# Kernel optimization log

Measured on AMD Instinct MI355X. Metric: run time of the kernel, lower is better.

## Reference

```python
import jax, jax.numpy as jnp
import numpy as np

N_NODE = 50000
N_EDGE = 625000
FDIM = 128
HID = 128
EPS = 1e-5


def setup_inputs() -> dict:
    key = jax.random.key(0)
    ks = jax.random.split(key, 12)
    node_feature = jax.random.normal(ks[0], (N_NODE, FDIM), dtype=jnp.float32)
    edge_matrix = jax.random.randint(ks[1], (2, N_EDGE), 0, N_NODE, dtype=jnp.int32)
    edge_feature = jax.random.normal(ks[2], (N_EDGE, FDIM), dtype=jnp.float32)
    in_dim = FDIM + FDIM  # concat(node, aggregated edge)
    s1 = 1.0 / np.sqrt(in_dim)
    s2 = 1.0 / np.sqrt(HID)
    W1 = jax.random.uniform(ks[3], (in_dim, HID), jnp.float32, -s1, s1)
    b1 = jax.random.uniform(ks[4], (HID,), jnp.float32, -s1, s1)
    W2 = jax.random.uniform(ks[5], (HID, HID), jnp.float32, -s2, s2)
    b2 = jax.random.uniform(ks[6], (HID,), jnp.float32, -s2, s2)
    W3 = jax.random.uniform(ks[7], (HID, FDIM), jnp.float32, -s2, s2)
    b3 = jax.random.uniform(ks[8], (FDIM,), jnp.float32, -s2, s2)
    gamma = jnp.ones((FDIM,), jnp.float32)
    beta = jnp.zeros((FDIM,), jnp.float32)
    return {"node_feature": node_feature, "edge_matrix": edge_matrix,
            "edge_feature": edge_feature, "W1": W1, "b1": b1, "W2": W2,
            "b2": b2, "W3": W3, "b3": b3, "gamma": gamma, "beta": beta}


def reference(node_feature, edge_matrix, edge_feature, W1, b1, W2, b2, W3, b3, gamma, beta):
    # receiver_idx = edge_matrix.T[:, 1] with edge_matrix [2, N_edge] -> row 1
    receiver_idx = edge_matrix[1]
    # scatter_add over receiver: [N_node, fdim]
    agg = jax.ops.segment_sum(edge_feature, receiver_idx, num_segments=node_feature.shape[0])
    x = jnp.concatenate([node_feature, agg], axis=-1)  # [N_node, 2*fdim]
    h = jax.nn.relu(x @ W1 + b1)
    h = jax.nn.relu(h @ W2 + b2)
    h = h @ W3 + b3
    # LayerNorm over last dim (eps = 1e-5, torch default)
    mu = jnp.mean(h, axis=-1, keepdims=True)
    var = jnp.mean((h - mu) ** 2, axis=-1, keepdims=True)
    h = (h - mu) * jax.lax.rsqrt(var + EPS) * gamma + beta
    return h + node_feature
```

## Files before the change

kernel.cpp:

```cpp
#include <hip/hip_runtime.h>
#include <hip/hip_bf16.h>

#define N_NODE 50000
#define N_EDGE 625000
#define FDIM 128
#define CAP 64

typedef __bf16 bf16x8 __attribute__((ext_vector_type(8)));
typedef float floatx4 __attribute__((ext_vector_type(4)));

#define MT 64
#define XS_LD 264
#define H_LD 136

__device__ inline bf16x8 as_bf16x8(uint4 v) {
    union { uint4 u; bf16x8 b; } c; c.u = v; return c.b;
}

__global__ __launch_bounds__(256) void wrepack_kernel(
    const float* __restrict__ W1, const float* __restrict__ W2,
    const float* __restrict__ W3, uint4* __restrict__ wp,
    int* __restrict__ count)
{
    if (blockIdx.x >= 32) {
        int idx = (blockIdx.x - 32) * 256 + threadIdx.x;
        for (int i = idx; i < N_NODE; i += 32 * 256) count[i] = 0;
        return;
    }
    int g = blockIdx.x * 256 + threadIdx.x;
    int lane = g & 63;
    int nt = (g >> 6) & 7;
    int tile = g >> 9;
    const float* W; int k0;
    if (tile < 8)       { W = W1; k0 = tile * 32; }
    else if (tile < 12) { W = W2; k0 = (tile - 8) * 32; }
    else                { W = W3; k0 = (tile - 12) * 32; }
    int n = nt * 16 + (lane & 15);
    int kb = k0 + (lane >> 4) * 8;
    union { __bf16 b[8]; uint4 u; } p;
#pragma unroll
    for (int j = 0; j < 8; ++j) p.b[j] = (__bf16)W[(kb + j) * 128 + n];
    wp[g] = p.u;
}

__global__ __launch_bounds__(256) void scatter_kernel(
    const int4* __restrict__ recv4, int* __restrict__ count, int* __restrict__ eid)
{
    int tid = blockIdx.x * 256 + threadIdx.x;
    if (tid < N_EDGE / 4) {
        int4 r = recv4[tid];
        int e0 = tid * 4;
        int p0 = atomicAdd(&count[r.x], 1);
        int p1 = atomicAdd(&count[r.y], 1);
        int p2 = atomicAdd(&count[r.z], 1);
        int p3 = atomicAdd(&count[r.w], 1);
        if (p0 < CAP) eid[(r.x << 6) + p0] = e0;
        if (p1 < CAP) eid[(r.y << 6) + p1] = e0 + 1;
        if (p2 < CAP) eid[(r.z << 6) + p2] = e0 + 2;
        if (p3 < CAP) eid[(r.w << 6) + p3] = e0 + 3;
    }
}

__global__ __launch_bounds__(256) void gather_kernel(
    const float4* __restrict__ ef4, const int* __restrict__ count,
    const int* __restrict__ eid, uint2* __restrict__ agg)
{
    int wave = threadIdx.x >> 6;
    int lane = threadIdx.x & 63;
    int node = blockIdx.x * 4 + wave;
    int half = lane >> 5;
    int c = lane & 31;
    float4 acc = {0.f, 0.f, 0.f, 0.f};
    int ids = eid[(node << 6) + lane];
    int cnt = count[node]; if (cnt > CAP) cnt = CAP;
    int j = 0;
    for (; j + 8 <= cnt; j += 8) {
        int ea = __shfl(ids, j + half);
        int eb = __shfl(ids, j + 2 + half);
        int ec = __shfl(ids, j + 4 + half);
        int ed = __shfl(ids, j + 6 + half);
        float4 va = ef4[(long)ea * 32 + c];
        float4 vb = ef4[(long)eb * 32 + c];
        float4 vc = ef4[(long)ec * 32 + c];
        float4 vd = ef4[(long)ed * 32 + c];
        acc.x += va.x + vb.x + vc.x + vd.x;
        acc.y += va.y + vb.y + vc.y + vd.y;
        acc.z += va.z + vb.z + vc.z + vd.z;
        acc.w += va.w + vb.w + vc.w + vd.w;
    }
    if (j + 4 <= cnt) {
        int ea = __shfl(ids, j + half);
        int eb = __shfl(ids, j + 2 + half);
        float4 va = ef4[(long)ea * 32 + c];
        float4 vb = ef4[(long)eb * 32 + c];
        acc.x += va.x + vb.x; acc.y += va.y + vb.y;
        acc.z += va.z + vb.z; acc.w += va.w + vb.w;
        j += 4;
    }
    if (j + 2 <= cnt) {
        int e = __shfl(ids, j + half);
        float4 v = ef4[(long)e * 32 + c];
        acc.x += v.x; acc.y += v.y; acc.z += v.z; acc.w += v.w;
        j += 2;
    }
    if (j + half < cnt) {
        int e = __shfl(ids, j + half);
        float4 v = ef4[(long)e * 32 + c];
        acc.x += v.x; acc.y += v.y; acc.z += v.z; acc.w += v.w;
    }
    acc.x += __shfl_xor(acc.x, 32);
    acc.y += __shfl_xor(acc.y, 32);
    acc.z += __shfl_xor(acc.z, 32);
    acc.w += __shfl_xor(acc.w, 32);
    if (half == 0) {
        union { __bf16 b[4]; uint2 u; } p;
        p.b[0] = (__bf16)acc.x; p.b[1] = (__bf16)acc.y;
        p.b[2] = (__bf16)acc.z; p.b[3] = (__bf16)acc.w;
        agg[(long)node * 32 + c] = p.u;
    }
}

__global__ __launch_bounds__(256, 4) void mlp_kernel(
    const float* __restrict__ nodef, const int* __restrict__ agg32,
    const uint4* __restrict__ wp,
    const float* __restrict__ b1, const float* __restrict__ b2,
    const float* __restrict__ b3,
    const float* __restrict__ gamma, const float* __restrict__ beta,
    float* __restrict__ out)
{
    __shared__ __bf16 smem[17472];
    __bf16* xs = smem;
    __bf16* h1 = smem;
    __bf16* h2 = smem + 8704;

    const int t = threadIdx.x;
    const int wave = t >> 6;
    const int lane = t & 63;
    const int quad = lane >> 4;
    const int l16 = lane & 15;
    const int w16 = wave << 4;
    const int q8 = quad << 3;
    const int node0 = blockIdx.x * MT;

    const float4* nf4 = (const float4*)nodef;
#pragma unroll
    for (int i = 0; i < 8; ++i) {
        int it = i * 256 + t;
        int row = it >> 5;
        int c4 = it & 31;
        int node = node0 + row;
        if (node >= N_NODE) node = N_NODE - 1;
        float4 v = nf4[(long)node * 32 + c4];
        union { __bf16 b[4]; short4 s; } u;
        u.b[0] = (__bf16)v.x; u.b[1] = (__bf16)v.y;
        u.b[2] = (__bf16)v.z; u.b[3] = (__bf16)v.w;
        *(short4*)&xs[row * XS_LD + c4 * 4] = u.s;
    }
    const int4* ag4 = (const int4*)agg32;
#pragma unroll
    for (int i = 0; i < 4; ++i) {
        int it = i * 256 + t;
        int row = it >> 4;
        int c8 = it & 15;
        int node = node0 + row;
        if (node >= N_NODE) node = N_NODE - 1;
        int4 v = ag4[(long)node * 16 + c8];
        *(int4*)&xs[row * XS_LD + 128 + c8 * 8] = v;
    }

    floatx4 acc[8];
    const floatx4 zero = {0.f, 0.f, 0.f, 0.f};

    auto run_gemm = [&](const __bf16* A, int ldA, const uint4* __restrict__ wpt, int nk) {
#pragma unroll
        for (int nt = 0; nt < 8; ++nt) acc[nt] = zero;
        const __bf16* arow = A + (w16 + l16) * ldA + q8;
        bf16x8 a = *(const bf16x8*)arow;
        bf16x8 bA[4], bB[4];
#pragma unroll
        for (int i = 0; i < 4; ++i) bA[i] = as_bf16x8(wpt[i * 64 + lane]);
        for (int kc = 0; kc < nk; ++kc) {
            const uint4* wk = wpt + kc * 512;
#pragma unroll
            for (int i = 0; i < 4; ++i) bB[i] = as_bf16x8(wk[(4 + i) * 64 + lane]);
            bf16x8 a2 = a;
            if (kc + 1 < nk) a2 = *(const bf16x8*)(arow + (kc + 1) * 32);
#pragma unroll
            for (int nt = 0; nt < 4; ++nt)
                acc[nt] = __builtin_amdgcn_mfma_f32_16x16x32_bf16(a, bA[nt], acc[nt], 0, 0, 0);
            if (kc + 1 < nk) {
#pragma unroll
                for (int i = 0; i < 4; ++i) bA[i] = as_bf16x8(wk[512 + i * 64 + lane]);
            }
#pragma unroll
            for (int nt = 0; nt < 4; ++nt)
                acc[4 + nt] = __builtin_amdgcn_mfma_f32_16x16x32_bf16(a, bB[nt], acc[4 + nt], 0, 0, 0);
            a = a2;
        }
    };

    auto epilogue_relu = [&](const float* __restrict__ bias, __bf16* H) {
#pragma unroll
        for (int nt = 0; nt < 8; ++nt) {
            int col = nt * 16 + l16;
            float bv = bias[col];
#pragma unroll
            for (int r = 0; r < 4; ++r) {
                float v = acc[nt][r] + bv;
                v = v > 0.f ? v : 0.f;
                H[(w16 + quad * 4 + r) * H_LD + col] = (__bf16)v;
            }
        }
    };

    __syncthreads();
    run_gemm(xs, XS_LD, wp, 8);
    __syncthreads();
    epilogue_relu(b1, h1);
    __syncthreads();
    run_gemm(h1, H_LD, wp + 4096, 4);
    epilogue_relu(b2, h2);
    __syncthreads();
    run_gemm(h2, H_LD, wp + 6144, 4);

    float vout[8][4];
    float sum[4] = {0.f, 0.f, 0.f, 0.f};
    float sq[4]  = {0.f, 0.f, 0.f, 0.f};
#pragma unroll
    for (int nt = 0; nt < 8; ++nt) {
        int col = nt * 16 + l16;
        float bv = b3[col];
#pragma unroll
        for (int r = 0; r < 4; ++r) {
            float v = acc[nt][r] + bv;
            vout[nt][r] = v;
            sum[r] += v;
            sq[r] += v * v;
        }
    }
#pragma unroll
    for (int r = 0; r < 4; ++r) {
#pragma unroll
        for (int offs = 1; offs < 16; offs <<= 1) {
            sum[r] += __shfl_xor(sum[r], offs);
            sq[r]  += __shfl_xor(sq[r], offs);
        }
    }
    float mu[4], rs[4];
#pragma unroll
    for (int r = 0; r < 4; ++r) {
        mu[r] = sum[r] * (1.f / 128.f);
        float var = sq[r] * (1.f / 128.f) - mu[r] * mu[r];
        rs[r] = rsqrtf(var + 1e-5f);
    }
#pragma unroll
    for (int nt = 0; nt < 8; ++nt) {
        int col = nt * 16 + l16;
        float g = gamma[col], be = beta[col];
#pragma unroll
        for (int r = 0; r < 4; ++r) {
            int row = w16 + quad * 4 + r;
            int node = node0 + row;
            if (node < N_NODE) {
                long o = (long)node * 128 + col;
                out[o] = (vout[nt][r] - mu[r]) * rs[r] * g + be + nodef[o];
            }
        }
    }
}

extern "C" void kernel_launch(void* const* d_in, const int* in_sizes, int n_in,
                              void* d_out, int out_size, void* d_ws, size_t ws_size,
                              hipStream_t stream)
{
    const float* nodef = (const float*)d_in[0];
    const int*   em    = (const int*)d_in[1];
    const float* ef    = (const float*)d_in[2];
    const float* W1    = (const float*)d_in[3];
    const float* b1    = (const float*)d_in[4];
    const float* W2    = (const float*)d_in[5];
    const float* b2    = (const float*)d_in[6];
    const float* W3    = (const float*)d_in[7];
    const float* b3    = (const float*)d_in[8];
    const float* gamma = (const float*)d_in[9];
    const float* beta  = (const float*)d_in[10];
    float* out = (float*)d_out;

    int* count = (int*)d_ws;
    int* agg32 = count + 50048;
    uint4* wp  = (uint4*)(agg32 + 3200000);

    int* eid = (int*)d_out;

    const int* recv = em + N_EDGE;

    wrepack_kernel<<<64, 256, 0, stream>>>(W1, W2, W3, wp, count);

    int sblocks = (N_EDGE / 4 + 255) / 256;
    scatter_kernel<<<sblocks, 256, 0, stream>>>((const int4*)recv, count, eid);
    gather_kernel<<<N_NODE / 4, 256, 0, stream>>>((const float4*)ef, count, eid, (uint2*)agg32);

    int mblocks = (N_NODE + MT - 1) / MT;
    mlp_kernel<<<mblocks, 256, 0, stream>>>(nodef, agg32, wp, b1, b2, b3,
                                            gamma, beta, out);
}
```

Before: 537.9 us.

## Halve MLP row tile and split output columns across wave pairs

The MLP kernel now processes 32 nodes per block instead of 64. Each pair of waves shares a 16-row tile, and each wave computes half of the 128 output columns. LayerNorm statistics are combined across the two waves through a small shared-memory reduction with an extra barrier. The aim is to cut per-block LDS and accumulator registers so more blocks fit and run, at the cost of reading weights from global/L2 twice as often per node and adding a sync.

```diff
diff --git a/kernel.cpp b/kernel.cpp
--- a/kernel.cpp
+++ b/kernel.cpp
@@ -9,7 +9,7 @@
 typedef __bf16 bf16x8 __attribute__((ext_vector_type(8)));
 typedef float floatx4 __attribute__((ext_vector_type(4)));
 
-#define MT 64
+#define MT 32
 #define XS_LD 264
 #define H_LD 136
 
@@ -120,7 +120,7 @@
     }
 }
 
-__global__ __launch_bounds__(256, 4) void mlp_kernel(
+__global__ __launch_bounds__(256, 5) void mlp_kernel(
     const float* __restrict__ nodef, const int* __restrict__ agg32,
     const uint4* __restrict__ wp,
     const float* __restrict__ b1, const float* __restrict__ b2,
@@ -128,23 +128,26 @@
     const float* __restrict__ gamma, const float* __restrict__ beta,
     float* __restrict__ out)
 {
-    __shared__ __bf16 smem[17472];
+    __shared__ __bf16 smem[8704];
+    __shared__ float red[2][32][2];
     __bf16* xs = smem;
     __bf16* h1 = smem;
-    __bf16* h2 = smem + 8704;
+    __bf16* h2 = smem + 4352;
 
     const int t = threadIdx.x;
     const int wave = t >> 6;
     const int lane = t & 63;
     const int quad = lane >> 4;
     const int l16 = lane & 15;
-    const int w16 = wave << 4;
+    const int tile = wave >> 1;
+    const int ch   = wave & 1;
+    const int trow = tile << 4;
     const int q8 = quad << 3;
     const int node0 = blockIdx.x * MT;
 
     const float4* nf4 = (const float4*)nodef;
 #pragma unroll
-    for (int i = 0; i < 8; ++i) {
+    for (int i = 0; i < 4; ++i) {
         int it = i * 256 + t;
         int row = it >> 5;
         int c4 = it & 31;
@@ -158,7 +161,7 @@
     }
     const int4* ag4 = (const int4*)agg32;
 #pragma unroll
-    for (int i = 0; i < 4; ++i) {
+    for (int i = 0; i < 2; ++i) {
         int it = i * 256 + t;
         int row = it >> 4;
         int c8 = it & 15;
@@ -168,47 +171,45 @@
         *(int4*)&xs[row * XS_LD + 128 + c8 * 8] = v;
     }
 
-    floatx4 acc[8];
+    floatx4 acc[4];
     const floatx4 zero = {0.f, 0.f, 0.f, 0.f};
 
     auto run_gemm = [&](const __bf16* A, int ldA, const uint4* __restrict__ wpt, int nk) {
 #pragma unroll
-        for (int nt = 0; nt < 8; ++nt) acc[nt] = zero;
-        const __bf16* arow = A + (w16 + l16) * ldA + q8;
+        for (int nt = 0; nt < 4; ++nt) acc[nt] = zero;
+        const __bf16* arow = A + (trow + l16) * ldA + q8;
+        const uint4* wc = wpt + (ch << 2) * 64;
         bf16x8 a = *(const bf16x8*)arow;
         bf16x8 bA[4], bB[4];
 #pragma unroll
-        for (int i = 0; i < 4; ++i) bA[i] = as_bf16x8(wpt[i * 64 + lane]);
+        for (int i = 0; i < 4; ++i) bA[i] = as_bf16x8(wc[i * 64 + lane]);
         for (int kc = 0; kc < nk; ++kc) {
-            const uint4* wk = wpt + kc * 512;
-#pragma unroll
-            for (int i = 0; i < 4; ++i) bB[i] = as_bf16x8(wk[(4 + i) * 64 + lane]);
             bf16x8 a2 = a;
-            if (kc + 1 < nk) a2 = *(const bf16x8*)(arow + (kc + 1) * 32);
+            if (kc + 1 < nk) {
+                const uint4* wn = wc + (kc + 1) * 512;
+#pragma unroll
+                for (int i = 0; i < 4; ++i) bB[i] = as_bf16x8(wn[i * 64 + lane]);
+                a2 = *(const bf16x8*)(arow + (kc + 1) * 32);
+            }
 #pragma unroll
             for (int nt = 0; nt < 4; ++nt)
                 acc[nt] = __builtin_amdgcn_mfma_f32_16x16x32_bf16(a, bA[nt], acc[nt], 0, 0, 0);
-            if (kc + 1 < nk) {
-#pragma unroll
-                for (int i = 0; i < 4; ++i) bA[i] = as_bf16x8(wk[512 + i * 64 + lane]);
-            }
-#pragma unroll
-            for (int nt = 0; nt < 4; ++nt)
-                acc[4 + nt] = __builtin_amdgcn_mfma_f32_16x16x32_bf16(a, bB[nt], acc[4 + nt], 0, 0, 0);
             a = a2;
+#pragma unroll
+            for (int i = 0; i < 4; ++i) bA[i] = bB[i];
         }
     };
 
     auto epilogue_relu = [&](const float* __restrict__ bias, __bf16* H) {
 #pragma unroll
-        for (int nt = 0; nt < 8; ++nt) {
-            int col = nt * 16 + l16;
+        for (int nt = 0; nt < 4; ++nt) {
+            int col = (ch << 6) + nt * 16 + l16;
             float bv = bias[col];
 #pragma unroll
             for (int r = 0; r < 4; ++r) {
                 float v = acc[nt][r] + bv;
                 v = v > 0.f ? v : 0.f;
-                H[(w16 + quad * 4 + r) * H_LD + col] = (__bf16)v;
+                H[(trow + quad * 4 + r) * H_LD + col] = (__bf16)v;
             }
         }
     };
@@ -223,12 +224,12 @@
     __syncthreads();
     run_gemm(h2, H_LD, wp + 6144, 4);
 
-    float vout[8][4];
+    float vout[4][4];
     float sum[4] = {0.f, 0.f, 0.f, 0.f};
     float sq[4]  = {0.f, 0.f, 0.f, 0.f};
 #pragma unroll
-    for (int nt = 0; nt < 8; ++nt) {
-        int col = nt * 16 + l16;
+    for (int nt = 0; nt < 4; ++nt) {
+        int col = (ch << 6) + nt * 16 + l16;
         float bv = b3[col];
 #pragma unroll
         for (int r = 0; r < 4; ++r) {
@@ -246,20 +247,31 @@
             sq[r]  += __shfl_xor(sq[r], offs);
         }
     }
+    if (l16 == 0) {
+#pragma unroll
+        for (int r = 0; r < 4; ++r) {
+            red[ch][trow + quad * 4 + r][0] = sum[r];
+            red[ch][trow + quad * 4 + r][1] = sq[r];
+        }
+    }
+    __syncthreads();
     float mu[4], rs[4];
 #pragma unroll
     for (int r = 0; r < 4; ++r) {
-        mu[r] = sum[r] * (1.f / 128.f);
-        float var = sq[r] * (1.f / 128.f) - mu[r] * mu[r];
+        int row = trow + quad * 4 + r;
+        float s = red[0][row][0] + red[1][row][0];
+        float q = red[0][row][1] + red[1][row][1];
+        mu[r] = s * (1.f / 128.f);
+        float var = q * (1.f / 128.f) - mu[r] * mu[r];
         rs[r] = rsqrtf(var + 1e-5f);
     }
 #pragma unroll
-    for (int nt = 0; nt < 8; ++nt) {
-        int col = nt * 16 + l16;
+    for (int nt = 0; nt < 4; ++nt) {
+        int col = (ch << 6) + nt * 16 + l16;
         float g = gamma[col], be = beta[col];
 #pragma unroll
         for (int r = 0; r < 4; ++r) {
-            int row = w16 + quad * 4 + r;
+            int row = trow + quad * 4 + r;
             int node = node0 + row;
             if (node < N_NODE) {
                 long o = (long)node * 128 + col;
```

Result: no change. 529.2 us, median of 2 (-1.6%).
